# Optimization experiments

Measured on AMD Instinct MI355X. Metric: run time of the kernel, lower is better.

## Reference

```python
import jax, jax.numpy as jnp
import numpy as np

EPS = 1e-6
DIM = 2048
N_HEADS = 16
HEAD_DIM = DIM // N_HEADS  # 128
SEQ = 1040
CACHE = 8320
BATCH = 1


def rms_norm(x, g):
    # RMSNorm over the full model dim (WanRMSNorm)
    var = jnp.mean(jnp.square(x.astype(jnp.float32)), axis=-1, keepdims=True)
    return (x.astype(jnp.float32) * jax.lax.rsqrt(var + EPS)).astype(x.dtype) * g


def rope_apply(x, freqs):
    # x: [b, s, n, d]; freqs: [s, d//2] rotation angles (complex rotation on interleaved pairs)
    b, s, n, d = x.shape
    xr = x.reshape(b, s, n, d // 2, 2)
    xe, xo = xr[..., 0], xr[..., 1]
    cos = jnp.cos(freqs)[None, :, None, :]  # [1, s, 1, d//2]
    sin = jnp.sin(freqs)[None, :, None, :]
    out = jnp.stack([xe * cos - xo * sin, xe * sin + xo * cos], axis=-1)
    return out.reshape(b, s, n, d)


def sdpa(q, k, v):
    # q: [b, sq, n, d]; k, v: [b, skv, n, d]
    d = q.shape[-1]
    scale = 1.0 / jnp.sqrt(jnp.asarray(d, dtype=q.dtype))
    scores = jnp.einsum('bqnd,bknd->bnqk', q, k) * scale
    p = jax.nn.softmax(scores, axis=-1)
    return jnp.einsum('bnqk,bknd->bqnd', p, v)


def setup_inputs() -> dict:
    key = jax.random.key(0)
    ks = jax.random.split(key, 16)
    sc = 1.0 / np.sqrt(DIM)
    inp = {
        'x': jax.random.normal(ks[0], (BATCH, SEQ, DIM), dtype=jnp.float32),
        'seq_lens': jnp.full((BATCH,), SEQ, dtype=jnp.int32),
        'freqs': jax.random.uniform(ks[1], (SEQ, HEAD_DIM // 2), dtype=jnp.float32, maxval=2 * np.pi),
        'kv_cache_k': jax.random.normal(ks[2], (BATCH, CACHE, N_HEADS, HEAD_DIM), dtype=jnp.float32),
        'kv_cache_v': jax.random.normal(ks[3], (BATCH, CACHE, N_HEADS, HEAD_DIM), dtype=jnp.float32),
        'Wq': jax.random.normal(ks[4], (DIM, DIM), dtype=jnp.float32) * sc,
        'bq': jnp.zeros((DIM,), dtype=jnp.float32),
        'Wk': jax.random.normal(ks[5], (DIM, DIM), dtype=jnp.float32) * sc,
        'bk': jnp.zeros((DIM,), dtype=jnp.float32),
        'Wv': jax.random.normal(ks[6], (DIM, DIM), dtype=jnp.float32) * sc,
        'bv': jnp.zeros((DIM,), dtype=jnp.float32),
        'Wo': jax.random.normal(ks[7], (DIM, DIM), dtype=jnp.float32) * sc,
        'bo': jnp.zeros((DIM,), dtype=jnp.float32),
        'g_q': jnp.ones((DIM,), dtype=jnp.float32),
        'g_k': jnp.ones((DIM,), dtype=jnp.float32),
        'kv_start': 0,
        'kv_len': CACHE,
    }
    return inp


def reference(x, seq_lens, freqs, kv_cache_k, kv_cache_v, Wq, bq, Wk, bk, Wv, bv, Wo, bo, g_q, g_k, kv_start, kv_len):
    b, s, dim = x.shape
    d = 2 * freqs.shape[-1]
    n = dim // d
    q = rms_norm(x @ Wq + bq, g_q).reshape(b, s, n, d)
    k = rms_norm(x @ Wk + bk, g_k).reshape(b, s, n, d)
    v = (x @ Wv + bv).reshape(b, s, n, d)
    rq = rope_apply(q, freqs)
    rk = rope_apply(k, freqs)
    # kv_size[1] > 0 branch: concat cached KV slice with the new chunk
    k_full = jnp.concatenate([kv_cache_k[:, kv_start:kv_start + kv_len], rk], axis=1)
    v_full = jnp.concatenate([kv_cache_v[:, kv_start:kv_start + kv_len], v], axis=1)
    o = sdpa(rq, k_full, v_full)  # [b, s, n, d]
    return o.reshape(b, s, n * d) @ Wo + bo
```

## Files before the change

### kernel.cpp

```cpp
#include <hip/hip_runtime.h>

using bf16x8 = __attribute__((ext_vector_type(8))) short;
using f32x4  = __attribute__((ext_vector_type(4))) float;

#define DEV static __device__ __forceinline__

constexpr int SEQ    = 1040;
constexpr int MDIM   = 2048;
constexpr int NH     = 16;
constexpr int HD     = 128;
constexpr int NCACHE = 8320;
constexpr int LTOT   = NCACHE + SEQ;
constexpr int NQT    = 17;
constexpr int NQT2   = 9;

DEV float b2f(unsigned short u) {
  union { unsigned int i; float f; } z; z.i = ((unsigned int)u) << 16; return z.f;
}
DEV unsigned short f2b(float f) {
  union { float f; unsigned int i; } z; z.f = f;
  return (unsigned short)((z.i + 0x7fffu + ((z.i >> 16) & 1u)) >> 16);
}
DEV unsigned int cvtpk(float lo, float hi) {
  unsigned int r;
  asm("v_cvt_pk_bf16_f32 %0, %1, %2" : "=v"(r) : "v"(lo), "v"(hi));
  return r;
}
union U4S8 { uint4 u; short s[8]; };

__global__ __launch_bounds__(256) void convx_k(
    const float* __restrict__ x, unsigned short* __restrict__ xb, int n8) {
  int i = blockIdx.x * 256 + threadIdx.x;
  if (i < n8) {
    const float* p = x + (size_t)i * 8;
    f32x4 a = *(const f32x4*)p, b = *(const f32x4*)(p + 4);
    uint4 u = make_uint4(cvtpk(a[0], a[1]), cvtpk(a[2], a[3]),
                         cvtpk(b[0], b[1]), cvtpk(b[2], b[3]));
    *(uint4*)(xb + (size_t)i * 8) = u;
  }
}

__global__ __launch_bounds__(256) void convt_k(
    const float* __restrict__ W0, const float* __restrict__ W1,
    const float* __restrict__ W2, const float* __restrict__ W3,
    unsigned short* __restrict__ T0, unsigned short* __restrict__ T1,
    unsigned short* __restrict__ T2, unsigned short* __restrict__ T3) {
  __shared__ short T[64][72];
  const int zz = blockIdx.z;
  const float* W = (zz == 0) ? W0 : (zz == 1) ? W1 : (zz == 2) ? W2 : W3;
  unsigned short* O = (zz == 0) ? T0 : (zz == 1) ? T1 : (zz == 2) ? T2 : T3;
  const int r0 = blockIdx.y * 64, c0 = blockIdx.x * 64;
  const int t = threadIdx.x;
  {
    int row = t >> 2, cq = t & 3;
    const float* p = W + (size_t)(r0 + row) * MDIM + c0 + cq * 16;
    f32x4 a = *(const f32x4*)(p);
    f32x4 b = *(const f32x4*)(p + 4);
    f32x4 c = *(const f32x4*)(p + 8);
    f32x4 d = *(const f32x4*)(p + 12);
    *(uint4*)&T[row][cq * 16] =
        make_uint4(cvtpk(a[0], a[1]), cvtpk(a[2], a[3]), cvtpk(b[0], b[1]), cvtpk(b[2], b[3]));
    *(uint4*)&T[row][cq * 16 + 8] =
        make_uint4(cvtpk(c[0], c[1]), cvtpk(c[2], c[3]), cvtpk(d[0], d[1]), cvtpk(d[2], d[3]));
  }
  __syncthreads();
  {
    int c = t >> 2, kq = t & 3;
    U4S8 v0, v1;
#pragma unroll
    for (int i = 0; i < 8; ++i) v0.s[i] = T[kq * 16 + i][c];
#pragma unroll
    for (int i = 0; i < 8; ++i) v1.s[i] = T[kq * 16 + 8 + i][c];
    unsigned short* op = O + (size_t)(c0 + c) * MDIM + r0 + kq * 16;
    *(uint4*)(op) = v0.u;
    *(uint4*)(op + 8) = v1.u;
  }
}

__global__ __launch_bounds__(256) void gemm_qkv_k(
    const unsigned short* __restrict__ xb,
    const unsigned short* __restrict__ Wtq, const unsigned short* __restrict__ Wtk,
    const unsigned short* __restrict__ Wtv,
    const float* __restrict__ bq, const float* __restrict__ bk, const float* __restrict__ bv,
    unsigned short* __restrict__ Qb, unsigned short* __restrict__ Kn, unsigned short* __restrict__ Vn) {
  __shared__ short As[64][72];
  __shared__ short Bs[128][72];
  const int tid = threadIdx.x;
  const int l = tid & 63, wv = tid >> 6;
  const int l16 = l & 15, kl = l >> 4;
  const int m0 = blockIdx.y * 64;
  const int n0g = blockIdx.x * 128;
  const int which = n0g >> 11;
  const int n0 = n0g & 2047;
  const unsigned short* Wt = (which == 0) ? Wtq : (which == 1) ? Wtk : Wtv;
  const float* bias = (which == 0) ? bq : (which == 1) ? bk : bv;
  unsigned short* outp = (which == 0) ? Qb : (which == 1) ? Kn : Vn;
  const int wm = (wv >> 1) * 32, wn = (wv & 1) * 64;
  f32x4 acc[2][4] = {};
  for (int k0 = 0; k0 < MDIM; k0 += 64) {
    {
      int m = tid >> 2, kq = tid & 3;
      int row = m0 + m;
      uint4 v0 = make_uint4(0, 0, 0, 0), v1 = make_uint4(0, 0, 0, 0);
      if (row < SEQ) {
        const unsigned short* p = xb + (size_t)row * MDIM + k0 + kq * 16;
        v0 = *(const uint4*)p;
        v1 = *(const uint4*)(p + 8);
      }
      *(uint4*)&As[m][kq * 16] = v0;
      *(uint4*)&As[m][kq * 16 + 8] = v1;
    }
    {
      int n = tid >> 1, kq = tid & 1;
      const unsigned short* p = Wt + (size_t)(n0 + n) * MDIM + k0 + kq * 32;
      uint4 v0 = *(const uint4*)p, v1 = *(const uint4*)(p + 8);
      uint4 v2 = *(const uint4*)(p + 16), v3 = *(const uint4*)(p + 24);
      *(uint4*)&Bs[n][kq * 32] = v0;
      *(uint4*)&Bs[n][kq * 32 + 8] = v1;
      *(uint4*)&Bs[n][kq * 32 + 16] = v2;
      *(uint4*)&Bs[n][kq * 32 + 24] = v3;
    }
    __syncthreads();
#pragma unroll
    for (int kk = 0; kk < 2; ++kk) {
      bf16x8 aF[2], bF[4];
#pragma unroll
      for (int mi = 0; mi < 2; ++mi)
        aF[mi] = *(const bf16x8*)&As[wm + mi * 16 + l16][kk * 32 + kl * 8];
#pragma unroll
      for (int ni = 0; ni < 4; ++ni)
        bF[ni] = *(const bf16x8*)&Bs[wn + ni * 16 + l16][kk * 32 + kl * 8];
#pragma unroll
      for (int mi = 0; mi < 2; ++mi)
#pragma unroll
        for (int ni = 0; ni < 4; ++ni)
          acc[mi][ni] = __builtin_amdgcn_mfma_f32_16x16x32_bf16(
              aF[mi], bF[ni], acc[mi][ni], 0, 0, 0);
    }
    __syncthreads();
  }
#pragma unroll
  for (int ni = 0; ni < 4; ++ni) {
    const int col = n0 + wn + ni * 16 + l16;
    const float bb = bias[col];
#pragma unroll
    for (int mi = 0; mi < 2; ++mi) {
      const int rowb = m0 + wm + mi * 16 + kl * 4;
#pragma unroll
      for (int r = 0; r < 4; ++r) {
        const int row = rowb + r;
        if (row >= SEQ) continue;
        outp[((size_t)(col >> 7) * SEQ + row) * HD + (col & 127)] = f2b(acc[mi][ni][r] + bb);
      }
    }
  }
}

__global__ __launch_bounds__(256) void gemm_o_k(
    const unsigned short* __restrict__ Ab, const unsigned short* __restrict__ Wt,
    const float* __restrict__ bias, float* __restrict__ outp) {
  __shared__ short As[64][72];
  __shared__ short Bs[128][72];
  const int tid = threadIdx.x;
  const int l = tid & 63, wv = tid >> 6;
  const int l16 = l & 15, kl = l >> 4;
  const int m0 = blockIdx.y * 64, n0 = blockIdx.x * 128;
  const int wm = (wv >> 1) * 32, wn = (wv & 1) * 64;
  f32x4 acc[2][4] = {};
  for (int k0 = 0; k0 < MDIM; k0 += 64) {
    {
      int m = tid >> 2, kq = tid & 3;
      int row = m0 + m, k = k0 + kq * 16;
      uint4 v0 = make_uint4(0, 0, 0, 0), v1 = make_uint4(0, 0, 0, 0);
      if (row < SEQ) {
        const unsigned short* p = Ab + ((size_t)(k >> 7) * SEQ + row) * HD + (k & 127);
        v0 = *(const uint4*)p;
        v1 = *(const uint4*)(p + 8);
      }
      *(uint4*)&As[m][kq * 16] = v0;
      *(uint4*)&As[m][kq * 16 + 8] = v1;
    }
    {
      int n = tid >> 1, kq = tid & 1;
      const unsigned short* p = Wt + (size_t)(n0 + n) * MDIM + k0 + kq * 32;
      uint4 v0 = *(const uint4*)p, v1 = *(const uint4*)(p + 8);
      uint4 v2 = *(const uint4*)(p + 16), v3 = *(const uint4*)(p + 24);
      *(uint4*)&Bs[n][kq * 32] = v0;
      *(uint4*)&Bs[n][kq * 32 + 8] = v1;
      *(uint4*)&Bs[n][kq * 32 + 16] = v2;
      *(uint4*)&Bs[n][kq * 32 + 24] = v3;
    }
    __syncthreads();
#pragma unroll
    for (int kk = 0; kk < 2; ++kk) {
      bf16x8 aF[2], bF[4];
#pragma unroll
      for (int mi = 0; mi < 2; ++mi)
        aF[mi] = *(const bf16x8*)&As[wm + mi * 16 + l16][kk * 32 + kl * 8];
#pragma unroll
      for (int ni = 0; ni < 4; ++ni)
        bF[ni] = *(const bf16x8*)&Bs[wn + ni * 16 + l16][kk * 32 + kl * 8];
#pragma unroll
      for (int mi = 0; mi < 2; ++mi)
#pragma unroll
        for (int ni = 0; ni < 4; ++ni)
          acc[mi][ni] = __builtin_amdgcn_mfma_f32_16x16x32_bf16(
              aF[mi], bF[ni], acc[mi][ni], 0, 0, 0);
    }
    __syncthreads();
  }
#pragma unroll
  for (int ni = 0; ni < 4; ++ni) {
    const int col = n0 + wn + ni * 16 + l16;
    const float bb = bias[col];
#pragma unroll
    for (int mi = 0; mi < 2; ++mi) {
      const int rowb = m0 + wm + mi * 16 + kl * 4;
#pragma unroll
      for (int r = 0; r < 4; ++r) {
        const int row = rowb + r;
        if (row >= SEQ) continue;
        outp[(size_t)row * MDIM + col] = acc[mi][ni][r] + bb;
      }
    }
  }
}

__global__ __launch_bounds__(256) void rmsrope_k(
    unsigned short* __restrict__ Qb, unsigned short* __restrict__ Kn,
    const float* __restrict__ gq, const float* __restrict__ gk,
    const float* __restrict__ fr) {
  const int s = blockIdx.x, which = blockIdx.y;
  unsigned short* B = which ? Kn : Qb;
  const float* g = which ? gk : gq;
  __shared__ float cs[64], sn[64], red[4];
  const int t = threadIdx.x;
  if (t < 64) {
    float a = fr[s * 64 + t];
    cs[t] = cosf(a);
    sn[t] = sinf(a);
  }
  const int c0 = t * 8;
  const int hh = c0 >> 7, dd = c0 & 127, p0 = dd >> 1;
  const size_t addr = ((size_t)hh * SEQ + s) * HD + dd;
  bf16x8 v = *(const bf16x8*)(B + addr);
  float y[8];
#pragma unroll
  for (int i = 0; i < 8; ++i) y[i] = b2f((unsigned short)v[i]);
  float ssq = 0.f;
#pragma unroll
  for (int i = 0; i < 8; ++i) ssq += y[i] * y[i];
#pragma unroll
  for (int off = 32; off; off >>= 1) ssq += __shfl_xor(ssq, off);
  if ((t & 63) == 0) red[t >> 6] = ssq;
  __syncthreads();
  const float var = (red[0] + red[1] + red[2] + red[3]) * (1.0f / MDIM);
  const float rs = rsqrtf(var + 1e-6f);
  bf16x8 ov;
#pragma unroll
  for (int i = 0; i < 4; ++i) {
    float e = b2f(f2b(y[2 * i] * rs)) * g[c0 + 2 * i];
    float o = b2f(f2b(y[2 * i + 1] * rs)) * g[c0 + 2 * i + 1];
    float C = cs[p0 + i], S = sn[p0 + i];
    ov[2 * i]     = (short)f2b(e * C - o * S);
    ov[2 * i + 1] = (short)f2b(e * S + o * C);
  }
  *(bf16x8*)(B + addr) = ov;
}

__global__ __launch_bounds__(512) void attn_part2_k(
    const unsigned short* __restrict__ Qb, const unsigned short* __restrict__ Kn,
    const unsigned short* __restrict__ Vn, const float* __restrict__ Kc,
    const float* __restrict__ Vc, float* __restrict__ Opart,
    float* __restrict__ ml, int chunk, int S) {
  __shared__ short UN[9216];
  __shared__ short Vt[128][72];
  const int b = blockIdx.x;
  const int xcd = b & 7;
  const int r_ = b >> 3;
  const int qt = r_ % NQT2;
  const int g = (r_ / NQT2) * 8 + xcd;
  const int h = g & (NH - 1);
  const int z = g >> 4;
  const int tid = threadIdx.x, wv = tid >> 6, l = tid & 63;
  const int l16 = l & 15, kl = l >> 4;
  const float SCALE = 0.08838834764831845f;

  const int c0 = z * chunk;
  const int cend = min(c0 + chunk, LTOT);

  int qrow = qt * 128 + wv * 16 + l16;
  if (qrow > SEQ - 1) qrow = SEQ - 1;
  bf16x8 qf[4];
#pragma unroll
  for (int kk = 0; kk < 4; ++kk)
    qf[kk] = *(const bf16x8*)(Qb + ((size_t)h * SEQ + qrow) * HD + kk * 32 + kl * 8);

  f32x4 oacc[8] = {};
  float mrow[4] = {-1e30f, -1e30f, -1e30f, -1e30f};
  float lrow[4] = {0.f, 0.f, 0.f, 0.f};

  for (int kv0 = c0; kv0 < cend; kv0 += 64) {
#pragma unroll
    for (int it = 0; it < 2; ++it) {
      int slot = tid + it * 512;
      int j = slot & 63, dq = slot >> 6;
      int jg = kv0 + j;
      U4S8 ku, vu;
      ku.u = make_uint4(0, 0, 0, 0);
      vu.u = make_uint4(0, 0, 0, 0);
      if (jg < NCACHE) {
        const float* kp = Kc + ((size_t)jg * NH + h) * HD + dq * 8;
        const float* vp = Vc + ((size_t)jg * NH + h) * HD + dq * 8;
        f32x4 ka = *(const f32x4*)(kp), kb = *(const f32x4*)(kp + 4);
        f32x4 va = *(const f32x4*)(vp), vb = *(const f32x4*)(vp + 4);
        ku.u = make_uint4(cvtpk(ka[0], ka[1]), cvtpk(ka[2], ka[3]),
                          cvtpk(kb[0], kb[1]), cvtpk(kb[2], kb[3]));
        vu.u = make_uint4(cvtpk(va[0], va[1]), cvtpk(va[2], va[3]),
                          cvtpk(vb[0], vb[1]), cvtpk(vb[2], vb[3]));
      } else if (jg < LTOT) {
        ku.u = *(const uint4*)(Kn + ((size_t)h * SEQ + (jg - NCACHE)) * HD + dq * 8);
        vu.u = *(const uint4*)(Vn + ((size_t)h * SEQ + (jg - NCACHE)) * HD + dq * 8);
      }
      *(uint4*)&UN[j * 136 + dq * 8] = ku.u;
#pragma unroll
      for (int i = 0; i < 8; ++i) Vt[dq * 8 + i][j] = vu.s[i];
    }
    __syncthreads();

    f32x4 sa[4] = {};
#pragma unroll
    for (int ni = 0; ni < 4; ++ni)
#pragma unroll
      for (int kk = 0; kk < 4; ++kk) {
        bf16x8 bK = *(const bf16x8*)&UN[(ni * 16 + l16) * 136 + kk * 32 + kl * 8];
        sa[ni] = __builtin_amdgcn_mfma_f32_16x16x32_bf16(qf[kk], bK, sa[ni], 0, 0, 0);
      }
    __syncthreads();

    float sv[4][4];
    float pm[4] = {-1e30f, -1e30f, -1e30f, -1e30f};
#pragma unroll
    for (int ni = 0; ni < 4; ++ni) {
      int jg = kv0 + ni * 16 + l16;
      bool valid = jg < LTOT;
#pragma unroll
      for (int r = 0; r < 4; ++r) {
        float xs = valid ? sa[ni][r] * SCALE : -1e30f;
        sv[ni][r] = xs;
        pm[r] = fmaxf(pm[r], xs);
      }
    }
#pragma unroll
    for (int off = 1; off < 16; off <<= 1)
#pragma unroll
      for (int r = 0; r < 4; ++r) pm[r] = fmaxf(pm[r], __shfl_xor(pm[r], off));

    float sc[4];
#pragma unroll
    for (int r = 0; r < 4; ++r) {
      float mn = fmaxf(mrow[r], pm[r]);
      sc[r] = __expf(mrow[r] - mn);
      mrow[r] = mn;
    }
    float ps[4] = {0.f, 0.f, 0.f, 0.f};
#pragma unroll
    for (int ni = 0; ni < 4; ++ni)
#pragma unroll
      for (int r = 0; r < 4; ++r) {
        float p = __expf(sv[ni][r] - mrow[r]);
        sv[ni][r] = p;
        ps[r] += p;
      }
#pragma unroll
    for (int off = 1; off < 16; off <<= 1)
#pragma unroll
      for (int r = 0; r < 4; ++r) ps[r] += __shfl_xor(ps[r], off);
#pragma unroll
    for (int r = 0; r < 4; ++r) lrow[r] = lrow[r] * sc[r] + ps[r];
#pragma unroll
    for (int di = 0; di < 8; ++di)
#pragma unroll
      for (int r = 0; r < 4; ++r) oacc[di][r] *= sc[r];
#pragma unroll
    for (int ni = 0; ni < 4; ++ni)
#pragma unroll
      for (int r = 0; r < 4; ++r)
        UN[(wv * 16 + kl * 4 + r) * 72 + ni * 16 + l16] = (short)f2b(sv[ni][r]);
    __syncthreads();

#pragma unroll
    for (int di = 0; di < 8; ++di)
#pragma unroll
      for (int k2 = 0; k2 < 2; ++k2) {
        bf16x8 aP = *(const bf16x8*)&UN[(wv * 16 + l16) * 72 + k2 * 32 + kl * 8];
        bf16x8 bV = *(const bf16x8*)&Vt[di * 16 + l16][k2 * 32 + kl * 8];
        oacc[di] = __builtin_amdgcn_mfma_f32_16x16x32_bf16(aP, bV, oacc[di], 0, 0, 0);
      }
    __syncthreads();
  }

  const size_t pbase = (((size_t)z * NH + h) * NQT2 + qt);
  const int row = wv * 16 + kl * 4;
#pragma unroll
  for (int r = 0; r < 4; ++r) {
    float* Op = Opart + (pbase * 128 + row + r) * HD;
#pragma unroll
    for (int di = 0; di < 8; ++di) Op[di * 16 + l16] = oacc[di][r];
    ml[(pbase * 2 + 0) * 128 + row + r] = mrow[r];
    ml[(pbase * 2 + 1) * 128 + row + r] = lrow[r];
  }
}

__global__ __launch_bounds__(512) void attn_merge2_k(
    const float* __restrict__ Opart, const float* __restrict__ ml,
    unsigned short* __restrict__ Qb, int S) {
  const int qt = blockIdx.x, h = blockIdx.y;
  const int t = threadIdx.x;
  const int row = t >> 2, d0 = (t & 3) * 32;
  const int q = qt * 128 + row;

  float M = -1e30f;
  for (int s = 0; s < S; ++s) {
    const size_t pbase = (((size_t)s * NH + h) * NQT2 + qt);
    M = fmaxf(M, ml[(pbase * 2 + 0) * 128 + row]);
  }
  float L = 0.f;
  float o[32];
#pragma unroll
  for (int i = 0; i < 32; ++i) o[i] = 0.f;
  for (int s = 0; s < S; ++s) {
    const size_t pbase = (((size_t)s * NH + h) * NQT2 + qt);
    const float ms = ml[(pbase * 2 + 0) * 128 + row];
    const float ls = ml[(pbase * 2 + 1) * 128 + row];
    const float w = __expf(ms - M);
    L += w * ls;
    const float* Op = Opart + (pbase * 128 + row) * HD + d0;
#pragma unroll
    for (int c = 0; c < 8; ++c) {
      f32x4 v = *(const f32x4*)(Op + c * 4);
#pragma unroll
      for (int i = 0; i < 4; ++i) o[c * 4 + i] += w * v[i];
    }
  }
  if (q < SEQ) {
    const float inv = 1.f / L;
    unsigned short* op = Qb + ((size_t)h * SEQ + q) * HD + d0;
#pragma unroll
    for (int i = 0; i < 32; ++i) op[i] = f2b(o[i] * inv);
  }
}

extern "C" void kernel_launch(void* const* d_in, const int* in_sizes, int n_in,
                              void* d_out, int out_size, void* d_ws, size_t ws_size,
                              hipStream_t stream) {
  const float* x  = (const float*)d_in[0];
  const float* fr = (const float*)d_in[2];
  const float* Kc = (const float*)d_in[3];
  const float* Vc = (const float*)d_in[4];
  const float* Wq = (const float*)d_in[5];
  const float* bq = (const float*)d_in[6];
  const float* Wk = (const float*)d_in[7];
  const float* bk = (const float*)d_in[8];
  const float* Wv = (const float*)d_in[9];
  const float* bv = (const float*)d_in[10];
  const float* Wo = (const float*)d_in[11];
  const float* bo = (const float*)d_in[12];
  const float* gq = (const float*)d_in[13];
  const float* gk = (const float*)d_in[14];

  unsigned short* xb  = (unsigned short*)d_ws;
  unsigned short* Wtq = xb + (size_t)SEQ * MDIM;
  unsigned short* Wtk = Wtq + (size_t)MDIM * MDIM;
  unsigned short* Wtv = Wtk + (size_t)MDIM * MDIM;
  unsigned short* Wto = Wtv + (size_t)MDIM * MDIM;
  unsigned short* Qb  = Wto + (size_t)MDIM * MDIM;
  unsigned short* Kn  = Qb + (size_t)NH * SEQ * HD;
  unsigned short* Vn  = Kn + (size_t)NH * SEQ * HD;
  const size_t baseB = ((size_t)SEQ * MDIM + 4 * (size_t)MDIM * MDIM
                        + 3 * (size_t)NH * SEQ * HD) * 2;

  const size_t perSplitB = (size_t)NH * NQT2 * 128 * HD * 4
                         + (size_t)NH * NQT2 * 2 * 128 * 4;
  int S = 0;
  if (ws_size >= baseB + 8 * perSplitB + (1 << 20)) S = 8;
  else if (ws_size >= baseB + 6 * perSplitB + (1 << 20)) S = 6;
  else if (ws_size >= baseB + 4 * perSplitB + (1 << 19)) S = 4;

  convx_k<<<dim3((SEQ * MDIM / 8 + 255) / 256), 256, 0, stream>>>(x, xb, SEQ * MDIM / 8);
  convt_k<<<dim3(32, 32, 4), 256, 0, stream>>>(Wq, Wk, Wv, Wo, Wtq, Wtk, Wtv, Wto);

  gemm_qkv_k<<<dim3(48, 17), 256, 0, stream>>>(xb, Wtq, Wtk, Wtv, bq, bk, bv, Qb, Kn, Vn);
  rmsrope_k<<<dim3(SEQ, 2), 256, 0, stream>>>(Qb, Kn, gq, gk, fr);

  float* Opart = (float*)((char*)d_ws + baseB);
  float* ml    = Opart + (size_t)S * NH * NQT2 * 128 * HD;
  const int tiles = (LTOT + 63) / 64;
  const int chunk = ((tiles + S - 1) / S) * 64;
  attn_part2_k<<<dim3(NQT2 * NH * S), 512, 0, stream>>>(Qb, Kn, Vn, Kc, Vc, Opart, ml, chunk, S);
  attn_merge2_k<<<dim3(NQT2, NH), 512, 0, stream>>>(Opart, ml, Qb, S);

  gemm_o_k<<<dim3(16, 17), 256, 0, stream>>>(Qb, Wto, bo, (float*)d_out);
}
```

Before: 429.8 us.

## Pre-convert KV cache to bf16 into unified buffer; store attention partials in bf16

Adds a kernel that converts the fp32 K/V cache to bf16 once into a row-major [rows, MDIM] buffer. The QKV GEMM and RMS/RoPE kernels now write the new K/V rows into that same buffer. The attention kernel then loads bf16 tiles directly, with no per-tile fp32 conversion or cache/new-chunk branching, which cuts the repeated fp32 cache reads done for every query tile. Split partial outputs are now stored as bf16 and placed in workspace aliased over the transposed Q weights, which halves partial traffic but adds rounding. The split count may now default to 4. The padded tail rows of the K/V buffer are never initialised, so they rely on masking in the attention kernel.

```diff
diff --git a/kernel.cpp b/kernel.cpp
--- a/kernel.cpp
+++ b/kernel.cpp
@@ -11,7 +11,7 @@
 constexpr int HD     = 128;
 constexpr int NCACHE = 8320;
 constexpr int LTOT   = NCACHE + SEQ;
-constexpr int NQT    = 17;
+constexpr int KROWS  = 9408;
 constexpr int NQT2   = 9;
 
 DEV float b2f(unsigned short u) {
@@ -37,6 +37,21 @@
     uint4 u = make_uint4(cvtpk(a[0], a[1]), cvtpk(a[2], a[3]),
                          cvtpk(b[0], b[1]), cvtpk(b[2], b[3]));
     *(uint4*)(xb + (size_t)i * 8) = u;
+  }
+}
+
+__global__ __launch_bounds__(256) void convkv_k(
+    const float* __restrict__ Kc, const float* __restrict__ Vc,
+    unsigned short* __restrict__ Kb, unsigned short* __restrict__ Vb, int n8) {
+  int i = blockIdx.x * 256 + threadIdx.x;
+  const float* src = blockIdx.y ? Vc : Kc;
+  unsigned short* dst = blockIdx.y ? Vb : Kb;
+  if (i < n8) {
+    const float* p = src + (size_t)i * 8;
+    f32x4 a = *(const f32x4*)p, b = *(const f32x4*)(p + 4);
+    uint4 u = make_uint4(cvtpk(a[0], a[1]), cvtpk(a[2], a[3]),
+                         cvtpk(b[0], b[1]), cvtpk(b[2], b[3]));
+    *(uint4*)(dst + (size_t)i * 8) = u;
   }
 }
 
@@ -82,7 +97,7 @@
     const unsigned short* __restrict__ Wtq, const unsigned short* __restrict__ Wtk,
     const unsigned short* __restrict__ Wtv,
     const float* __restrict__ bq, const float* __restrict__ bk, const float* __restrict__ bv,
-    unsigned short* __restrict__ Qb, unsigned short* __restrict__ Kn, unsigned short* __restrict__ Vn) {
+    unsigned short* __restrict__ Qb, unsigned short* __restrict__ Kb, unsigned short* __restrict__ Vb) {
   __shared__ short As[64][72];
   __shared__ short Bs[128][72];
   const int tid = threadIdx.x;
@@ -94,7 +109,6 @@
   const int n0 = n0g & 2047;
   const unsigned short* Wt = (which == 0) ? Wtq : (which == 1) ? Wtk : Wtv;
   const float* bias = (which == 0) ? bq : (which == 1) ? bk : bv;
-  unsigned short* outp = (which == 0) ? Qb : (which == 1) ? Kn : Vn;
   const int wm = (wv >> 1) * 32, wn = (wv & 1) * 64;
   f32x4 acc[2][4] = {};
   for (int k0 = 0; k0 < MDIM; k0 += 64) {
@@ -150,7 +164,14 @@
       for (int r = 0; r < 4; ++r) {
         const int row = rowb + r;
         if (row >= SEQ) continue;
-        outp[((size_t)(col >> 7) * SEQ + row) * HD + (col & 127)] = f2b(acc[mi][ni][r] + bb);
+        const unsigned short val = f2b(acc[mi][ni][r] + bb);
+        if (which == 0) {
+          Qb[((size_t)(col >> 7) * SEQ + row) * HD + (col & 127)] = val;
+        } else if (which == 1) {
+          Kb[(size_t)(NCACHE + row) * MDIM + col] = val;
+        } else {
+          Vb[(size_t)(NCACHE + row) * MDIM + col] = val;
+        }
       }
     }
   }
@@ -227,11 +248,10 @@
 }
 
 __global__ __launch_bounds__(256) void rmsrope_k(
-    unsigned short* __restrict__ Qb, unsigned short* __restrict__ Kn,
+    unsigned short* __restrict__ Qb, unsigned short* __restrict__ Kb,
     const float* __restrict__ gq, const float* __restrict__ gk,
     const float* __restrict__ fr) {
   const int s = blockIdx.x, which = blockIdx.y;
-  unsigned short* B = which ? Kn : Qb;
   const float* g = which ? gk : gq;
   __shared__ float cs[64], sn[64], red[4];
   const int t = threadIdx.x;
@@ -242,8 +262,10 @@
   }
   const int c0 = t * 8;
   const int hh = c0 >> 7, dd = c0 & 127, p0 = dd >> 1;
-  const size_t addr = ((size_t)hh * SEQ + s) * HD + dd;
-  bf16x8 v = *(const bf16x8*)(B + addr);
+  unsigned short* ptr = which
+      ? Kb + (size_t)(NCACHE + s) * MDIM + c0
+      : Qb + ((size_t)hh * SEQ + s) * HD + dd;
+  bf16x8 v = *(const bf16x8*)ptr;
   float y[8];
 #pragma unroll
   for (int i = 0; i < 8; ++i) y[i] = b2f((unsigned short)v[i]);
@@ -265,13 +287,12 @@
     ov[2 * i]     = (short)f2b(e * C - o * S);
     ov[2 * i + 1] = (short)f2b(e * S + o * C);
   }
-  *(bf16x8*)(B + addr) = ov;
-}
-
-__global__ __launch_bounds__(512) void attn_part2_k(
-    const unsigned short* __restrict__ Qb, const unsigned short* __restrict__ Kn,
-    const unsigned short* __restrict__ Vn, const float* __restrict__ Kc,
-    const float* __restrict__ Vc, float* __restrict__ Opart,
+  *(bf16x8*)ptr = ov;
+}
+
+__global__ __launch_bounds__(512) void attn_part6_k(
+    const unsigned short* __restrict__ Qb, const unsigned short* __restrict__ Kb,
+    const unsigned short* __restrict__ Vb, unsigned short* __restrict__ Opart,
     float* __restrict__ ml, int chunk, int S) {
   __shared__ short UN[9216];
   __shared__ short Vt[128][72];
@@ -300,31 +321,19 @@
   float mrow[4] = {-1e30f, -1e30f, -1e30f, -1e30f};
   float lrow[4] = {0.f, 0.f, 0.f, 0.f};
 
+  const int j0 = tid & 63, dq0 = tid >> 6, dq1 = (tid + 512) >> 6;
+  const int hofs = h * HD;
+
   for (int kv0 = c0; kv0 < cend; kv0 += 64) {
+    const size_t rbase = (size_t)(kv0 + j0) * MDIM + hofs;
 #pragma unroll
     for (int it = 0; it < 2; ++it) {
-      int slot = tid + it * 512;
-      int j = slot & 63, dq = slot >> 6;
-      int jg = kv0 + j;
-      U4S8 ku, vu;
-      ku.u = make_uint4(0, 0, 0, 0);
-      vu.u = make_uint4(0, 0, 0, 0);
-      if (jg < NCACHE) {
-        const float* kp = Kc + ((size_t)jg * NH + h) * HD + dq * 8;
-        const float* vp = Vc + ((size_t)jg * NH + h) * HD + dq * 8;
-        f32x4 ka = *(const f32x4*)(kp), kb = *(const f32x4*)(kp + 4);
-        f32x4 va = *(const f32x4*)(vp), vb = *(const f32x4*)(vp + 4);
-        ku.u = make_uint4(cvtpk(ka[0], ka[1]), cvtpk(ka[2], ka[3]),
-                          cvtpk(kb[0], kb[1]), cvtpk(kb[2], kb[3]));
-        vu.u = make_uint4(cvtpk(va[0], va[1]), cvtpk(va[2], va[3]),
-                          cvtpk(vb[0], vb[1]), cvtpk(vb[2], vb[3]));
-      } else if (jg < LTOT) {
-        ku.u = *(const uint4*)(Kn + ((size_t)h * SEQ + (jg - NCACHE)) * HD + dq * 8);
-        vu.u = *(const uint4*)(Vn + ((size_t)h * SEQ + (jg - NCACHE)) * HD + dq * 8);
-      }
-      *(uint4*)&UN[j * 136 + dq * 8] = ku.u;
-#pragma unroll
-      for (int i = 0; i < 8; ++i) Vt[dq * 8 + i][j] = vu.s[i];
+      const int dq = (it == 0) ? dq0 : dq1;
+      uint4 ku = *(const uint4*)(Kb + rbase + dq * 8);
+      U4S8 vu; vu.u = *(const uint4*)(Vb + rbase + dq * 8);
+      *(uint4*)&UN[j0 * 136 + dq * 8] = ku;
+#pragma unroll
+      for (int i = 0; i < 8; ++i) Vt[dq * 8 + i][j0] = vu.s[i];
     }
     __syncthreads();
 
@@ -404,16 +413,16 @@
   const int row = wv * 16 + kl * 4;
 #pragma unroll
   for (int r = 0; r < 4; ++r) {
-    float* Op = Opart + (pbase * 128 + row + r) * HD;
-#pragma unroll
-    for (int di = 0; di < 8; ++di) Op[di * 16 + l16] = oacc[di][r];
+    unsigned short* Op = Opart + (pbase * 128 + row + r) * HD;
+#pragma unroll
+    for (int di = 0; di < 8; ++di) Op[di * 16 + l16] = f2b(oacc[di][r]);
     ml[(pbase * 2 + 0) * 128 + row + r] = mrow[r];
     ml[(pbase * 2 + 1) * 128 + row + r] = lrow[r];
   }
 }
 
-__global__ __launch_bounds__(512) void attn_merge2_k(
-    const float* __restrict__ Opart, const float* __restrict__ ml,
+__global__ __launch_bounds__(512) void attn_merge3_k(
+    const unsigned short* __restrict__ Opart, const float* __restrict__ ml,
     unsigned short* __restrict__ Qb, int S) {
   const int qt = blockIdx.x, h = blockIdx.y;
   const int t = threadIdx.x;
@@ -435,12 +444,12 @@
     const float ls = ml[(pbase * 2 + 1) * 128 + row];
     const float w = __expf(ms - M);
     L += w * ls;
-    const float* Op = Opart + (pbase * 128 + row) * HD + d0;
-#pragma unroll
-    for (int c = 0; c < 8; ++c) {
-      f32x4 v = *(const f32x4*)(Op + c * 4);
-#pragma unroll
-      for (int i = 0; i < 4; ++i) o[c * 4 + i] += w * v[i];
+    const unsigned short* Op = Opart + (pbase * 128 + row) * HD + d0;
+#pragma unroll
+    for (int c = 0; c < 4; ++c) {
+      bf16x8 v = *(const bf16x8*)(Op + c * 8);
+#pragma unroll
+      for (int i = 0; i < 8; ++i) o[c * 8 + i] += w * b2f((unsigned short)v[i]);
     }
   }
   if (q < SEQ) {
@@ -470,35 +479,38 @@
   const float* gk = (const float*)d_in[14];
 
   unsigned short* xb  = (unsigned short*)d_ws;
-  unsigned short* Wtq = xb + (size_t)SEQ * MDIM;
+  unsigned short* Wto = xb + (size_t)SEQ * MDIM;
+  unsigned short* Qb  = Wto + (size_t)MDIM * MDIM;
+  unsigned short* Kb  = Qb + (size_t)NH * SEQ * HD;
+  unsigned short* Vb  = Kb + (size_t)KROWS * MDIM;
+  unsigned short* Wtq = Vb + (size_t)KROWS * MDIM;
   unsigned short* Wtk = Wtq + (size_t)MDIM * MDIM;
   unsigned short* Wtv = Wtk + (size_t)MDIM * MDIM;
-  unsigned short* Wto = Wtv + (size_t)MDIM * MDIM;
-  unsigned short* Qb  = Wto + (size_t)MDIM * MDIM;
-  unsigned short* Kn  = Qb + (size_t)NH * SEQ * HD;
-  unsigned short* Vn  = Kn + (size_t)NH * SEQ * HD;
-  const size_t baseB = ((size_t)SEQ * MDIM + 4 * (size_t)MDIM * MDIM
-                        + 3 * (size_t)NH * SEQ * HD) * 2;
-
-  const size_t perSplitB = (size_t)NH * NQT2 * 128 * HD * 4
+  const size_t fixedB = ((size_t)SEQ * MDIM + (size_t)MDIM * MDIM + (size_t)NH * SEQ * HD
+                         + 2 * (size_t)KROWS * MDIM) * 2;
+  const size_t aliasB = 3 * (size_t)MDIM * MDIM * 2;
+
+  const size_t perSplitB = (size_t)NH * NQT2 * 128 * HD * 2
                          + (size_t)NH * NQT2 * 2 * 128 * 4;
-  int S = 0;
-  if (ws_size >= baseB + 8 * perSplitB + (1 << 20)) S = 8;
-  else if (ws_size >= baseB + 6 * perSplitB + (1 << 20)) S = 6;
-  else if (ws_size >= baseB + 4 * perSplitB + (1 << 19)) S = 4;
-
-  convx_k<<<dim3((SEQ * MDIM / 8 + 255) / 256), 256, 0, stream>>>(x, xb, SEQ * MDIM / 8);
+  int S = 4;
+  if (ws_size >= fixedB + aliasB + (8 * perSplitB - aliasB) + (1 << 21)) S = 8;
+
+  unsigned short* Opart = Wtq;
+  float* ml = (float*)((char*)Wtq + (size_t)S * NH * NQT2 * 128 * HD * 2);
+
+  const int n8x = SEQ * MDIM / 8;
+  const int n8kv = NCACHE * MDIM / 8;
+  convx_k<<<dim3((n8x + 255) / 256), 256, 0, stream>>>(x, xb, n8x);
+  convkv_k<<<dim3((n8kv + 255) / 256, 2), 256, 0, stream>>>(Kc, Vc, Kb, Vb, n8kv);
   convt_k<<<dim3(32, 32, 4), 256, 0, stream>>>(Wq, Wk, Wv, Wo, Wtq, Wtk, Wtv, Wto);
 
-  gemm_qkv_k<<<dim3(48, 17), 256, 0, stream>>>(xb, Wtq, Wtk, Wtv, bq, bk, bv, Qb, Kn, Vn);
-  rmsrope_k<<<dim3(SEQ, 2), 256, 0, stream>>>(Qb, Kn, gq, gk, fr);
-
-  float* Opart = (float*)((char*)d_ws + baseB);
-  float* ml    = Opart + (size_t)S * NH * NQT2 * 128 * HD;
+  gemm_qkv_k<<<dim3(48, 17), 256, 0, stream>>>(xb, Wtq, Wtk, Wtv, bq, bk, bv, Qb, Kb, Vb);
+  rmsrope_k<<<dim3(SEQ, 2), 256, 0, stream>>>(Qb, Kb, gq, gk, fr);
+
   const int tiles = (LTOT + 63) / 64;
   const int chunk = ((tiles + S - 1) / S) * 64;
-  attn_part2_k<<<dim3(NQT2 * NH * S), 512, 0, stream>>>(Qb, Kn, Vn, Kc, Vc, Opart, ml, chunk, S);
-  attn_merge2_k<<<dim3(NQT2, NH), 512, 0, stream>>>(Opart, ml, Qb, S);
+  attn_part6_k<<<dim3(NQT2 * NH * S), 512, 0, stream>>>(Qb, Kb, Vb, Opart, ml, chunk, S);
+  attn_merge3_k<<<dim3(NQT2, NH), 512, 0, stream>>>(Opart, ml, Qb, S);
 
   gemm_o_k<<<dim3(16, 17), 256, 0, stream>>>(Qb, Wto, bo, (float*)d_out);
 }
```

Result: faster. 410.4 us (-4.5%).
